# Kernel tuning notes

Hardware: AMD Instinct MI355X
Metric: run time of the kernel (lower is better)

## Reference

```python
import jax, jax.numpy as jnp
import numpy as np

B, L, DM, H = 16, 2048, 1024, 16
DK = DM // H
FACTOR = 1


def setup_inputs() -> dict:
    key = jax.random.key(0)
    ks = jax.random.split(key, 8)
    s = 0.02
    return {
        "queries": jax.random.normal(ks[0], (B, L, DM), jnp.float32),
        "keys": jax.random.normal(ks[1], (B, L, DM), jnp.float32),
        "values": jax.random.normal(ks[2], (B, L, DM), jnp.float32),
        "Wq": jax.random.normal(ks[3], (DM, DM), jnp.float32) * s,
        "Wk": jax.random.normal(ks[4], (DM, DM), jnp.float32) * s,
        "Wv": jax.random.normal(ks[5], (DM, DM), jnp.float32) * s,
        "Wo": jax.random.normal(ks[6], (DM, DM), jnp.float32) * s,
        "bo": jnp.zeros((DM,), jnp.float32),
    }


def reference(queries, keys, values, Wq, Wk, Wv, Wo, bo):
    # Projections (torch Linear: y = x @ W.T), then [B, H, DK, L] layout
    Q = (queries @ Wq.T).reshape(B, L, H, DK).transpose(0, 2, 3, 1)
    K = (keys @ Wk.T).reshape(B, L, H, DK).transpose(0, 2, 3, 1)
    V = (values @ Wv.T).reshape(B, L, H, DK).transpose(0, 2, 3, 1)

    # FFT cross-correlation along time
    qf = jnp.fft.rfft(Q, axis=-1)
    kf = jnp.fft.rfft(K, axis=-1)
    corr = jnp.fft.irfft(qf * jnp.conj(kf), n=L, axis=-1)  # [B, H, DK, L]

    # time_delay_agg_inference (eval path); B == H so torch's right-aligned
    # broadcast maps the batch axis of delay/weights onto the HEAD axis.
    top_k = int(FACTOR * np.log(L))
    mean_value = jnp.mean(corr, axis=1)                     # [B, DK, L]
    weights, delay = jax.lax.top_k(mean_value, top_k)       # [B, DK, K]
    w = jax.nn.softmax(weights, axis=-1)

    pos = jnp.arange(L)
    agg = jnp.zeros_like(V)
    for i in range(top_k):  # small fixed loop (top_k = 7)
        idx = (pos[None, None, :] + delay[:, :, i][:, :, None]) % L  # first axis aligns with H
        pattern = jnp.take_along_axis(V, jnp.broadcast_to(idx[None], V.shape), axis=-1)
        agg = agg + pattern * w[:, :, i][None, :, :, None]

    out = agg.transpose(0, 3, 1, 2).reshape(B, L, DM)  # [B, L, H*DK]
    out = out @ Wo.T + bo
    return out, corr
```

## Files before the change

### kernel.cpp

```cpp
#include <hip/hip_runtime.h>
#include <hip/hip_fp16.h>
#include <hip/hip_bf16.h>
#include <cstdint>
#include <cstddef>

typedef float  f32x4 __attribute__((ext_vector_type(4)));
typedef short  s16x8 __attribute__((ext_vector_type(8)));
typedef unsigned short u16;
typedef unsigned int   u32;
typedef u32 u32x4 __attribute__((ext_vector_type(4)));
typedef u32 u32x2 __attribute__((ext_vector_type(2)));

#define TOPK 7

__device__ __forceinline__ u32 bfpk(float re, float im) {
  __hip_bfloat162 h = __float22bfloat162_rn(make_float2(re, im));
  return *(u32*)&h;
}
__device__ __forceinline__ u16 f2bf(float f) {
  __hip_bfloat16 h = __float2bfloat16(f);
  return *(u16*)&h;
}
__device__ __forceinline__ float b2f(u16 s) {
  return __uint_as_float(((u32)s) << 16);
}
__device__ __forceinline__ float2 bfup(u32 p) {
  float2 r; r.x = b2f((u16)(p & 0xffffu)); r.y = b2f((u16)(p >> 16)); return r;
}
__device__ __forceinline__ u32 pkf16(float c, float s) {
  __half2 h = __floats2half2_rn(c, s);
  return *(u32*)&h;
}
__device__ __forceinline__ float2 upf16(u32 p) {
  __half2 h; *(u32*)&h = p;
  float2 r; r.x = __low2float(h); r.y = __high2float(h); return r;
}

typedef __attribute__((address_space(1))) void gvoid;
typedef __attribute__((address_space(3))) void lvoid;
__device__ __forceinline__ void gl_lds16(const void* g, void* l) {
  __builtin_amdgcn_global_load_lds((gvoid*)g, (lvoid*)l, 16, 0, 0);
}

__global__ void cvt_kernel(const float* __restrict__ src, u16* __restrict__ dst, int n8) {
  int i = blockIdx.x * 256 + threadIdx.x;
  if (i >= n8) return;
  const f32x4* sp = (const f32x4*)src + (size_t)i * 2;
  f32x4 a = sp[0], b = sp[1];
  u32x4 o;
  o[0] = bfpk(a[0], a[1]); o[1] = bfpk(a[2], a[3]);
  o[2] = bfpk(b[0], b[1]); o[3] = bfpk(b[2], b[3]);
  *(u32x4*)(dst + (size_t)i * 8) = o;
}

template<int MODE>
__global__ __launch_bounds__(256, 2) void gemm_bt(
    const void* __restrict__ Aptr, const u16* __restrict__ Bw,
    void* __restrict__ Cout, const float* __restrict__ bias)
{
  constexpr int K = 1024, N = 1024;
  __shared__ __align__(16) u16 lA[2][128 * 32];
  __shared__ __align__(16) u16 lB[2][128 * 32];

  int bx = blockIdx.x;
  int wg = (bx & 7) * 256 + (bx >> 3);
  int tm = wg >> 3, tn = wg & 7;
  int m0 = tm * 128, n0 = tn * 128;

  int t = threadIdx.x;
  int wid = t >> 6, lane = t & 63;
  int wm = wid >> 1, wn = wid & 1;
  int lr = lane & 15, kb = lane >> 4;

  const float* A32 = (const float*)Aptr;
  const u16*   A16 = (const u16*)Aptr;
  int r = t >> 1, half = t & 1;

  f32x4 acc[4][4] = {};

  if constexpr (MODE == 0) {
    const float* ap = A32 + (size_t)(m0 + r) * K + half * 16;
    f32x4 v[4];
#pragma unroll
    for (int g = 0; g < 4; ++g) v[g] = ((const f32x4*)ap)[g];
    u32x4 o0, o1;
    o0[0] = bfpk(v[0][0], v[0][1]); o0[1] = bfpk(v[0][2], v[0][3]);
    o0[2] = bfpk(v[1][0], v[1][1]); o0[3] = bfpk(v[1][2], v[1][3]);
    o1[0] = bfpk(v[2][0], v[2][1]); o1[1] = bfpk(v[2][2], v[2][3]);
    o1[2] = bfpk(v[3][0], v[3][1]); o1[3] = bfpk(v[3][2], v[3][3]);
    *(u32x4*)&lA[0][r * 32 + half * 16]     = o0;
    *(u32x4*)&lA[0][r * 32 + half * 16 + 8] = o1;
  } else {
#pragma unroll
    for (int it = 0; it < 2; ++it) {
      int e = (t * 16 + it * 4096) >> 1;
      gl_lds16(A16 + (size_t)(m0 + (e >> 5)) * K + (e & 31),
               (char*)&lA[0][0] + wid * 1024 + it * 4096);
    }
  }
#pragma unroll
  for (int it = 0; it < 2; ++it) {
    int e = (t * 16 + it * 4096) >> 1;
    gl_lds16(Bw + (size_t)(n0 + (e >> 5)) * K + (e & 31),
             (char*)&lB[0][0] + wid * 1024 + it * 4096);
  }
  __syncthreads();

  int cur = 0;
  for (int kt = 0; kt < 32; ++kt) {
    int nxt = cur ^ 1;
    bool pf = (kt < 31);
    f32x4 va[4];
    if (pf) {
      int k1 = (kt + 1) * 32;
      if constexpr (MODE == 0) {
        const float* ap = A32 + (size_t)(m0 + r) * K + k1 + half * 16;
#pragma unroll
        for (int g = 0; g < 4; ++g) va[g] = ((const f32x4*)ap)[g];
      } else {
#pragma unroll
        for (int it = 0; it < 2; ++it) {
          int e = (t * 16 + it * 4096) >> 1;
          gl_lds16(A16 + (size_t)(m0 + (e >> 5)) * K + k1 + (e & 31),
                   (char*)&lA[nxt][0] + wid * 1024 + it * 4096);
        }
      }
#pragma unroll
      for (int it = 0; it < 2; ++it) {
        int e = (t * 16 + it * 4096) >> 1;
        gl_lds16(Bw + (size_t)(n0 + (e >> 5)) * K + k1 + (e & 31),
                 (char*)&lB[nxt][0] + wid * 1024 + it * 4096);
      }
    }
    s16x8 af[4], bf[4];
#pragma unroll
    for (int mi = 0; mi < 4; ++mi)
      af[mi] = *(const s16x8*)&lA[cur][(wm * 64 + mi * 16 + lr) * 32 + kb * 8];
#pragma unroll
    for (int ni = 0; ni < 4; ++ni)
      bf[ni] = *(const s16x8*)&lB[cur][(wn * 64 + ni * 16 + lr) * 32 + kb * 8];
#pragma unroll
    for (int mi = 0; mi < 4; ++mi)
#pragma unroll
      for (int ni = 0; ni < 4; ++ni)
        acc[mi][ni] = __builtin_amdgcn_mfma_f32_16x16x32_bf16(af[mi], bf[ni], acc[mi][ni], 0, 0, 0);
    if (pf) {
      if constexpr (MODE == 0) {
        u32x4 o0, o1;
        o0[0] = bfpk(va[0][0], va[0][1]); o0[1] = bfpk(va[0][2], va[0][3]);
        o0[2] = bfpk(va[1][0], va[1][1]); o0[3] = bfpk(va[1][2], va[1][3]);
        o1[0] = bfpk(va[2][0], va[2][1]); o1[1] = bfpk(va[2][2], va[2][3]);
        o1[2] = bfpk(va[3][0], va[3][1]); o1[3] = bfpk(va[3][2], va[3][3]);
        *(u32x4*)&lA[nxt][r * 32 + half * 16]     = o0;
        *(u32x4*)&lA[nxt][r * 32 + half * 16 + 8] = o1;
      }
    }
    __syncthreads();
    cur = nxt;
  }

#pragma unroll
  for (int mi = 0; mi < 4; ++mi) {
    int mbase = m0 + wm * 64 + mi * 16 + kb * 4;
#pragma unroll
    for (int ni = 0; ni < 4; ++ni) {
      int nn = n0 + wn * 64 + ni * 16 + lr;
      if constexpr (MODE == 0) {
        u16* OT = (u16*)Cout;
        int b = mbase >> 11, l = mbase & 2047;
        u32x2 pk;
        pk[0] = bfpk(acc[mi][ni][0], acc[mi][ni][1]);
        pk[1] = bfpk(acc[mi][ni][2], acc[mi][ni][3]);
        *(u32x2*)(OT + ((size_t)((b << 10) + nn)) * 2048 + l) = pk;
      } else {
        float* C = (float*)Cout;
        float bv = bias[nn];
#pragma unroll
        for (int j = 0; j < 4; ++j)
          C[(size_t)(mbase + j) * N + nn] = acc[mi][ni][j] + bv;
      }
    }
  }
}


__device__ __constant__ const int BRv[32] = {
  0,16,8,24,4,20,12,28,2,18,10,26,6,22,14,30,
  1,17,9,25,5,21,13,29,3,19,11,27,7,23,15,31};
__device__ const float C32v[16] = {
  1.0f, 0.98078528f, 0.92387953f, 0.83146961f,
  0.70710678f, 0.55557023f, 0.38268343f, 0.19509032f,
  0.0f, -0.19509032f, -0.38268343f, -0.55557023f,
  -0.70710678f, -0.83146961f, -0.92387953f, -0.98078528f};
__device__ const float S32v[16] = {
  0.0f, 0.19509032f, 0.38268343f, 0.55557023f,
  0.70710678f, 0.83146961f, 0.92387953f, 0.98078528f,
  1.0f, 0.98078528f, 0.92387953f, 0.83146961f,
  0.70710678f, 0.55557023f, 0.38268343f, 0.19509032f};

#define TWIDX(j) ((j) + ((j) >> 4))

template<bool INV>
__device__ __forceinline__ void dft32(float* xr, float* xi) {
#pragma unroll
  for (int s = 0; s < 5; ++s) {
    const int half = 1 << s, step = 16 >> s;
#pragma unroll
    for (int blk = 0; blk < 32; blk += 2 * half) {
#pragma unroll
      for (int j = 0; j < half; ++j) {
        float wr = C32v[j * step];
        float wi = INV ? S32v[j * step] : -S32v[j * step];
        int p = blk + j, q = p + half;
        float vr = xr[q] * wr - xi[q] * wi;
        float vi = xr[q] * wi + xi[q] * wr;
        xr[q] = xr[p] - vr; xi[q] = xi[p] - vi;
        xr[p] = xr[p] + vr; xi[p] = xi[p] + vi;
      }
    }
  }
}

__device__ __forceinline__ void fft_fwd_row(const u32* __restrict__ zrow, int tt,
                                            u32* wsr, const u32* twp,
                                            float* xr, float* xi) {
#pragma unroll
  for (int i = 0; i < 32; ++i) {
    float2 v = bfup(zrow[32 * BRv[i] + tt]);
    xr[i] = v.x; xi[i] = v.y;
  }
  dft32<false>(xr, xi);
#pragma unroll
  for (int k1 = 0; k1 < 32; ++k1) {
    float2 w = upf16(twp[TWIDX(tt * k1)]);
    wsr[k1 * 33 + tt] = bfpk(xr[k1] * w.x - xi[k1] * w.y,
                             xr[k1] * w.y + xi[k1] * w.x);
  }
  __syncthreads();
#pragma unroll
  for (int i = 0; i < 32; ++i) {
    float2 v = bfup(wsr[tt * 33 + BRv[i]]);
    xr[i] = v.x; xi[i] = v.y;
  }
  __syncthreads();
  dft32<false>(xr, xi);
}

__device__ __forceinline__ void spec_bin(
    float zlQr, float zlQi, float zpQr, float zpQi,
    float zlKr, float zlKi, float zpKr, float zpKi,
    float wr, float wi, float& outr, float& outi)
{
  float aQr = zlQr + zpQr, aQi = zlQi - zpQi;
  float bQr = zlQr - zpQr, bQi = zlQi + zpQi;
  float gQr  = aQr + wr * bQi + wi * bQr;
  float gQi  = aQi - (wr * bQr - wi * bQi);
  float gQpr = aQr - wr * bQi - wi * bQr;
  float gQpi = -aQi - wr * bQr + wi * bQi;
  float aKr = zlKr + zpKr, aKi = zlKi - zpKi;
  float bKr = zlKr - zpKr, bKi = zlKi + zpKi;
  float gKr  = aKr + wr * bKi + wi * bKr;
  float gKi  = aKi - (wr * bKr - wi * bKi);
  float gKpr = aKr - wr * bKi - wi * bKr;
  float gKpi = -aKi - wr * bKr + wi * bKi;
  float ctr = gQr * gKr + gQi * gKi;
  float cti = gQi * gKr - gQr * gKi;
  float cpr = gQpr * gKpr + gQpi * gKpi;
  float cpi = gQpi * gKpr - gQpr * gKpi;
  float utr = ctr + cpr, uti = cti - cpi;
  float vtr = ctr - cpr, vti = cti + cpi;
  outr = (utr - wr * vti + wi * vtr) * (1.0f / 8192.0f);
  outi = (uti + wr * vtr + wi * vti) * (1.0f / 8192.0f);
}

__global__ __launch_bounds__(256) void fftcorr_kernel(
    const u16* __restrict__ Qt, const u16* __restrict__ Kt, float* __restrict__ corr)
{
  __shared__ u32 twp[1088];
  __shared__ u32 wsb[8][1056];

  int t = threadIdx.x;
#pragma unroll
  for (int i = 0; i < 4; ++i) {
    int j = t + 256 * i;
    float s, c;
    __sincosf((float)j * -6.135923151e-3f, &s, &c);
    twp[TWIDX(j)] = pkf16(c, s);
  }
  __syncthreads();

  int rl = t >> 5, tt = t & 31;
  int row = blockIdx.x * 8 + rl;
  const u32* qrow = (const u32*)Qt + (size_t)row * 1024;
  const u32* krow = (const u32*)Kt + (size_t)row * 1024;
  u32* wsr = wsb[rl];
  int lw = t & 63;
  int paddr = (((-tt) & 31) | (lw & 32)) << 2;
  bool f0 = (tt == 0);

  float xr[32], xi[32];
  u32 zkp[32], ap[32], zcp[32];

  fft_fwd_row(krow, tt, wsr, twp, xr, xi);
#pragma unroll
  for (int i = 0; i < 32; ++i) zkp[i] = bfpk(xr[i], xi[i]);
  fft_fwd_row(qrow, tt, wsr, twp, xr, xi);
#pragma unroll
  for (int i = 0; i < 32; ++i) ap[i] = bfpk(xr[i], xi[i]);

#pragma unroll
  for (int j = 0; j < 16; ++j) {
    u32 qpA = (u32)__builtin_amdgcn_ds_bpermute(paddr, (int)ap[31 - j]);
    u32 kpA = (u32)__builtin_amdgcn_ds_bpermute(paddr, (int)zkp[31 - j]);
    u32 qpB = (u32)__builtin_amdgcn_ds_bpermute(paddr, (int)ap[j]);
    u32 kpB = (u32)__builtin_amdgcn_ds_bpermute(paddr, (int)zkp[j]);
    if (f0) {
      qpA = ap[(32 - j) & 31];  kpA = zkp[(32 - j) & 31];
      qpB = ap[(j + 1) & 31];   kpB = zkp[(j + 1) & 31];
    }
    float2 bA = upf16(twp[TWIDX((tt >> 1) + 16 * j)]);
    float2 bB = upf16(twp[TWIDX((tt >> 1) + 16 * (31 - j))]);
    bool oddk = (tt & 1);
    float mr = oddk ? 0.999995293810f : 1.0f;
    float mi = oddk ? -3.067956763e-3f : 0.0f;
    float wAr = bA.x * mr - bA.y * mi, wAi = bA.x * mi + bA.y * mr;
    float wBr = bB.x * mr - bB.y * mi, wBi = bB.x * mi + bB.y * mr;
    float2 zl, zp, kl, kp;
    float or_, oi_;
    zl = bfup(ap[j]);      zp = bfup(qpA);
    kl = bfup(zkp[j]);     kp = bfup(kpA);
    spec_bin(zl.x, zl.y, zp.x, zp.y, kl.x, kl.y, kp.x, kp.y, wAr, wAi, or_, oi_);
    zcp[j] = bfpk(or_, oi_);
    zl = bfup(ap[31 - j]); zp = bfup(qpB);
    kl = bfup(zkp[31 - j]); kp = bfup(kpB);
    spec_bin(zl.x, zl.y, zp.x, zp.y, kl.x, kl.y, kp.x, kp.y, wBr, wBi, or_, oi_);
    zcp[31 - j] = bfpk(or_, oi_);
  }

#define SWPU(a, b) { u32 tp = zcp[a]; zcp[a] = zcp[b]; zcp[b] = tp; }
  SWPU(1, 16) SWPU(2, 8) SWPU(3, 24) SWPU(5, 20) SWPU(6, 12) SWPU(7, 28)
  SWPU(9, 18) SWPU(11, 26) SWPU(13, 22) SWPU(15, 30) SWPU(19, 25) SWPU(23, 29)
#undef SWPU
#pragma unroll
  for (int i = 0; i < 32; ++i) {
    float2 v = bfup(zcp[i]);
    xr[i] = v.x; xi[i] = v.y;
  }
  dft32<true>(xr, xi);
#pragma unroll
  for (int v1 = 0; v1 < 32; ++v1) {
    float2 w = upf16(twp[TWIDX(tt * v1)]);
    wsr[v1 * 33 + tt] = bfpk(xr[v1] * w.x + xi[v1] * w.y,
                             xi[v1] * w.x - xr[v1] * w.y);
  }
  __syncthreads();
#pragma unroll
  for (int i = 0; i < 32; ++i) {
    float2 v = bfup(wsr[tt * 33 + BRv[i]]);
    xr[i] = v.x; xi[i] = v.y;
  }
  dft32<true>(xr, xi);

  float2* crow = (float2*)(corr + (size_t)row * 2048);
#pragma unroll
  for (int v2 = 0; v2 < 32; ++v2) {
    float2 o; o.x = xr[v2]; o.y = xi[v2];
    crow[tt + 32 * v2] = o;
  }
}

__global__ void mean_kernel(const float* __restrict__ corr, float* __restrict__ meanp) {
  int idx = blockIdx.x * 256 + threadIdx.x;
  int l4 = idx & 511;
  int d  = (idx >> 9) & 63;
  int b  = idx >> 15;
  const f32x4* cp = (const f32x4*)corr;
  f32x4 s = {};
#pragma unroll
  for (int h = 0; h < 16; ++h)
    s += cp[((size_t)(b * 1024 + h * 64 + d)) * 512 + l4];
  ((f32x4*)meanp)[(size_t)(b * 64 + d) * 512 + l4] = s * 0.0625f;
}

__global__ __launch_bounds__(256) void topk_kernel(
    const float* __restrict__ meanp, int* __restrict__ delays, float* __restrict__ wts)
{
  int row = blockIdx.x;
  const float* mr = meanp + (size_t)row * 2048;
  int t = threadIdx.x;
  float v[8];
#pragma unroll
  for (int j = 0; j < 8; ++j) v[j] = mr[t * 8 + j];
  __shared__ float sV[256];
  __shared__ int   sI[256];
  __shared__ float topv[TOPK];
  __shared__ int   topi[TOPK];
  for (int rnd = 0; rnd < TOPK; ++rnd) {
    float bv = v[0]; int bi = t * 8;
#pragma unroll
    for (int j = 1; j < 8; ++j)
      if (v[j] > bv) { bv = v[j]; bi = t * 8 + j; }
    sV[t] = bv; sI[t] = bi;
    __syncthreads();
    for (int off = 128; off > 0; off >>= 1) {
      if (t < off) {
        float ov = sV[t + off]; int oi = sI[t + off];
        if (ov > sV[t] || (ov == sV[t] && oi < sI[t])) { sV[t] = ov; sI[t] = oi; }
      }
      __syncthreads();
    }
    int wi = sI[0];
    if (t == 0) { topv[rnd] = sV[0]; topi[rnd] = wi; }
    if ((wi >> 3) == t) {
#pragma unroll
      for (int j = 0; j < 8; ++j)
        if ((wi & 7) == j) v[j] = -__builtin_inff();
    }
    __syncthreads();
  }
  if (t == 0) {
    float mx = topv[0], sum = 0.f, e[TOPK];
#pragma unroll
    for (int i = 0; i < TOPK; ++i) { e[i] = expf(topv[i] - mx); sum += e[i]; }
#pragma unroll
    for (int i = 0; i < TOPK; ++i) {
      wts[row * 8 + i]    = e[i] / sum;
      delays[row * 8 + i] = topi[i];
    }
  }
}

__global__ __launch_bounds__(256) void agg_kernel(
    const u16* __restrict__ Vt, const float* __restrict__ wts,
    const int* __restrict__ delays, u16* __restrict__ aggt)
{
  int row = blockIdx.x;
  int c = row & 1023;
  __shared__ __align__(16) float Vs[4608];
  __shared__ float wsh[TOPK];
  __shared__ int   dsh[TOPK];
  int t = threadIdx.x;
  if (t < TOPK) { wsh[t] = wts[c * 8 + t]; dsh[t] = delays[c * 8 + t]; }
  const u16* vr = Vt + (size_t)row * 2048;
  u32x4 rv = *(const u32x4*)(vr + t * 8);
  alignas(16) u16 uv[8];
  *(u32x4*)uv = rv;
  int f0 = t * 8;
#pragma unroll
  for (int j = 0; j < 8; ++j) {
    float fv = b2f(uv[j]);
    int f  = f0 + j;
    int f2 = f + 2048;
    Vs[f  + ((f  >> 5) << 2)] = fv;
    Vs[f2 + ((f2 >> 5) << 2)] = fv;
  }
  __syncthreads();
  float o[8] = {0, 0, 0, 0, 0, 0, 0, 0};
#pragma unroll
  for (int i = 0; i < TOPK; ++i) {
    float w = wsh[i]; int dl = dsh[i];
    int base = f0 + dl;
#pragma unroll
    for (int j = 0; j < 8; ++j) {
      int f = base + j;
      o[j] += w * Vs[f + ((f >> 5) << 2)];
    }
  }
  u32x4 ob;
  ob[0] = bfpk(o[0], o[1]); ob[1] = bfpk(o[2], o[3]);
  ob[2] = bfpk(o[4], o[5]); ob[3] = bfpk(o[6], o[7]);
  *(u32x4*)(aggt + (size_t)row * 2048 + f0) = ob;
}

__global__ __launch_bounds__(256) void transpose_kernel(
    const u16* __restrict__ aggt, u16* __restrict__ aggb)
{
  int bid = blockIdx.x;
  int lt = bid & 31;
  int ct = (bid >> 5) & 15;
  int b  = bid >> 9;
  __shared__ __align__(16) u16 tile[64][72];
  int t = threadIdx.x;
  int r = t >> 2, seg = t & 3;
  const u16* src = aggt + ((size_t)(b * 1024 + ct * 64 + r)) * 2048 + lt * 64 + seg * 16;
  u32x4 v0 = *(const u32x4*)src;
  u32x4 v1 = *(const u32x4*)(src + 8);
  *(u32x4*)&tile[r][seg * 16]     = v0;
  *(u32x4*)&tile[r][seg * 16 + 8] = v1;
  __syncthreads();
  alignas(16) u16 tmp[16];
#pragma unroll
  for (int j = 0; j < 16; ++j) tmp[j] = tile[seg * 16 + j][r];
  u16* dst = aggb + ((size_t)(b * 2048 + lt * 64 + r)) * 1024 + ct * 64 + seg * 16;
  *(u32x4*)dst       = *(u32x4*)&tmp[0];
  *(u32x4*)(dst + 8) = *(u32x4*)&tmp[8];
}

extern "C" void kernel_launch(void* const* d_in, const int* in_sizes, int n_in,
                              void* d_out, int out_size, void* d_ws, size_t ws_size,
                              hipStream_t stream) {
  (void)in_sizes; (void)n_in; (void)out_size; (void)ws_size;
  const float* qin = (const float*)d_in[0];
  const float* kin = (const float*)d_in[1];
  const float* vin = (const float*)d_in[2];
  const float* Wq  = (const float*)d_in[3];
  const float* Wk  = (const float*)d_in[4];
  const float* Wv  = (const float*)d_in[5];
  const float* Wo  = (const float*)d_in[6];
  const float* bo  = (const float*)d_in[7];

  float* out  = (float*)d_out;
  float* corr = out + (size_t)33554432;

  char* ws = (char*)d_ws;
  u16* Qt  = (u16*)ws;
  u16* Kt  = (u16*)(ws + ((size_t)64  << 20));
  u16* Vt  = (u16*)(ws + ((size_t)128 << 20));
  u16* Wqb = (u16*)(ws + ((size_t)192 << 20));
  u16* Wkb = Wqb + (1u << 20);
  u16* Wvb = Wkb + (1u << 20);
  u16* Wob = Wvb + (1u << 20);
  float* meanp  = (float*)(ws + ((size_t)200 << 20));
  int*   delays = (int*)  (ws + ((size_t)208 << 20));
  float* wts    = (float*)(ws + ((size_t)208 << 20) + 65536);
  u16* aggt = Qt;
  u16* aggb = Kt;

  dim3 blk(256);
  cvt_kernel<<<512, blk, 0, stream>>>(Wq, Wqb, 131072);
  cvt_kernel<<<512, blk, 0, stream>>>(Wk, Wkb, 131072);
  cvt_kernel<<<512, blk, 0, stream>>>(Wv, Wvb, 131072);
  cvt_kernel<<<512, blk, 0, stream>>>(Wo, Wob, 131072);

  gemm_bt<0><<<2048, blk, 0, stream>>>(qin, Wqb, Qt, nullptr);
  gemm_bt<0><<<2048, blk, 0, stream>>>(kin, Wkb, Kt, nullptr);
  gemm_bt<0><<<2048, blk, 0, stream>>>(vin, Wvb, Vt, nullptr);

  fftcorr_kernel<<<2048, blk, 0, stream>>>(Qt, Kt, corr);
  mean_kernel<<<2048, blk, 0, stream>>>(corr, meanp);
  topk_kernel<<<1024, blk, 0, stream>>>(meanp, delays, wts);
  agg_kernel<<<16384, blk, 0, stream>>>(Vt, wts, delays, aggt);
  transpose_kernel<<<8192, blk, 0, stream>>>(aggt, aggb);
  gemm_bt<1><<<2048, blk, 0, stream>>>(aggb, Wob, out, bo);
}
```

Before: 762.5 us.

## Triple-buffer GEMM LDS tiles with two-stage prefetch and manual waitcnt barriers

The projection/output GEMM moves from double- to triple-buffered LDS tiles and prefetches the k-tile two iterations ahead instead of one. `__syncthreads` is replaced by explicit `s_waitcnt` vmcnt/lgkmcnt plus a raw `s_barrier`, so the newest async global-to-LDS loads can stay in flight across the barrier. Load address offsets are also hoisted out of the loop. This aims to hide more global-memory latency behind MFMA work. The cost is 50% more LDS per block, which may limit occupancy, and hand-tuned wait counts that are fragile if the compiler reorders loads.

After: 793.1 us. 1.04x slower.

```diff
diff --git a/kernel.cpp b/kernel.cpp
--- a/kernel.cpp
+++ b/kernel.cpp
@@ -59,8 +59,8 @@
     void* __restrict__ Cout, const float* __restrict__ bias)
 {
   constexpr int K = 1024, N = 1024;
-  __shared__ __align__(16) u16 lA[2][128 * 32];
-  __shared__ __align__(16) u16 lB[2][128 * 32];
+  __shared__ __align__(16) u16 lA[3][128 * 32];
+  __shared__ __align__(16) u16 lB[3][128 * 32];
 
   int bx = blockIdx.x;
   int wg = (bx & 7) * 256 + (bx >> 3);
@@ -76,61 +76,67 @@
   const u16*   A16 = (const u16*)Aptr;
   int r = t >> 1, half = t & 1;
 
+  int e0 = (t * 16) >> 1;
+  int e1 = (t * 16 + 4096) >> 1;
+  int er0 = e0 >> 5, ec0 = e0 & 31;
+  int er1 = e1 >> 5, ec1 = e1 & 31;
+
   f32x4 acc[4][4] = {};
 
+#pragma unroll
+  for (int pt = 0; pt < 2; ++pt) {
+    int k0 = pt * 32;
+    if constexpr (MODE == 0) {
+      const float* ap = A32 + (size_t)(m0 + r) * K + k0 + half * 16;
+      f32x4 v[4];
+#pragma unroll
+      for (int g = 0; g < 4; ++g) v[g] = ((const f32x4*)ap)[g];
+      u32x4 o0, o1;
+      o0[0] = bfpk(v[0][0], v[0][1]); o0[1] = bfpk(v[0][2], v[0][3]);
+      o0[2] = bfpk(v[1][0], v[1][1]); o0[3] = bfpk(v[1][2], v[1][3]);
+      o1[0] = bfpk(v[2][0], v[2][1]); o1[1] = bfpk(v[2][2], v[2][3]);
+      o1[2] = bfpk(v[3][0], v[3][1]); o1[3] = bfpk(v[3][2], v[3][3]);
+      *(u32x4*)&lA[pt][r * 32 + half * 16]     = o0;
+      *(u32x4*)&lA[pt][r * 32 + half * 16 + 8] = o1;
+    } else {
+      gl_lds16(A16 + (size_t)(m0 + er0) * K + k0 + ec0,
+               (char*)&lA[pt][0] + wid * 1024);
+      gl_lds16(A16 + (size_t)(m0 + er1) * K + k0 + ec1,
+               (char*)&lA[pt][0] + wid * 1024 + 4096);
+    }
+    gl_lds16(Bw + (size_t)(n0 + er0) * K + k0 + ec0,
+             (char*)&lB[pt][0] + wid * 1024);
+    gl_lds16(Bw + (size_t)(n0 + er1) * K + k0 + ec1,
+             (char*)&lB[pt][0] + wid * 1024 + 4096);
+  }
   if constexpr (MODE == 0) {
-    const float* ap = A32 + (size_t)(m0 + r) * K + half * 16;
-    f32x4 v[4];
-#pragma unroll
-    for (int g = 0; g < 4; ++g) v[g] = ((const f32x4*)ap)[g];
-    u32x4 o0, o1;
-    o0[0] = bfpk(v[0][0], v[0][1]); o0[1] = bfpk(v[0][2], v[0][3]);
-    o0[2] = bfpk(v[1][0], v[1][1]); o0[3] = bfpk(v[1][2], v[1][3]);
-    o1[0] = bfpk(v[2][0], v[2][1]); o1[1] = bfpk(v[2][2], v[2][3]);
-    o1[2] = bfpk(v[3][0], v[3][1]); o1[3] = bfpk(v[3][2], v[3][3]);
-    *(u32x4*)&lA[0][r * 32 + half * 16]     = o0;
-    *(u32x4*)&lA[0][r * 32 + half * 16 + 8] = o1;
+    asm volatile("s_waitcnt vmcnt(2) lgkmcnt(0)" ::: "memory");
   } else {
-#pragma unroll
-    for (int it = 0; it < 2; ++it) {
-      int e = (t * 16 + it * 4096) >> 1;
-      gl_lds16(A16 + (size_t)(m0 + (e >> 5)) * K + (e & 31),
-               (char*)&lA[0][0] + wid * 1024 + it * 4096);
-    }
-  }
-#pragma unroll
-  for (int it = 0; it < 2; ++it) {
-    int e = (t * 16 + it * 4096) >> 1;
-    gl_lds16(Bw + (size_t)(n0 + (e >> 5)) * K + (e & 31),
-             (char*)&lB[0][0] + wid * 1024 + it * 4096);
-  }
-  __syncthreads();
+    asm volatile("s_waitcnt vmcnt(4) lgkmcnt(0)" ::: "memory");
+  }
+  __builtin_amdgcn_s_barrier();
 
   int cur = 0;
   for (int kt = 0; kt < 32; ++kt) {
-    int nxt = cur ^ 1;
-    bool pf = (kt < 31);
+    int wb = cur + 2; if (wb >= 3) wb -= 3;
+    bool pf2 = (kt < 30);
     f32x4 va[4];
-    if (pf) {
-      int k1 = (kt + 1) * 32;
+    if (pf2) {
+      int k2 = (kt + 2) * 32;
       if constexpr (MODE == 0) {
-        const float* ap = A32 + (size_t)(m0 + r) * K + k1 + half * 16;
+        const float* ap = A32 + (size_t)(m0 + r) * K + k2 + half * 16;
 #pragma unroll
         for (int g = 0; g < 4; ++g) va[g] = ((const f32x4*)ap)[g];
       } else {
-#pragma unroll
-        for (int it = 0; it < 2; ++it) {
-          int e = (t * 16 + it * 4096) >> 1;
-          gl_lds16(A16 + (size_t)(m0 + (e >> 5)) * K + k1 + (e & 31),
-                   (char*)&lA[nxt][0] + wid * 1024 + it * 4096);
-        }
+        gl_lds16(A16 + (size_t)(m0 + er0) * K + k2 + ec0,
+                 (char*)&lA[wb][0] + wid * 1024);
+        gl_lds16(A16 + (size_t)(m0 + er1) * K + k2 + ec1,
+                 (char*)&lA[wb][0] + wid * 1024 + 4096);
       }
-#pragma unroll
-      for (int it = 0; it < 2; ++it) {
-        int e = (t * 16 + it * 4096) >> 1;
-        gl_lds16(Bw + (size_t)(n0 + (e >> 5)) * K + k1 + (e & 31),
-                 (char*)&lB[nxt][0] + wid * 1024 + it * 4096);
-      }
+      gl_lds16(Bw + (size_t)(n0 + er0) * K + k2 + ec0,
+               (char*)&lB[wb][0] + wid * 1024);
+      gl_lds16(Bw + (size_t)(n0 + er1) * K + k2 + ec1,
+               (char*)&lB[wb][0] + wid * 1024 + 4096);
     }
     s16x8 af[4], bf[4];
 #pragma unroll
@@ -144,19 +150,27 @@
 #pragma unroll
       for (int ni = 0; ni < 4; ++ni)
         acc[mi][ni] = __builtin_amdgcn_mfma_f32_16x16x32_bf16(af[mi], bf[ni], acc[mi][ni], 0, 0, 0);
-    if (pf) {
+    if (pf2) {
       if constexpr (MODE == 0) {
         u32x4 o0, o1;
         o0[0] = bfpk(va[0][0], va[0][1]); o0[1] = bfpk(va[0][2], va[0][3]);
         o0[2] = bfpk(va[1][0], va[1][1]); o0[3] = bfpk(va[1][2], va[1][3]);
         o1[0] = bfpk(va[2][0], va[2][1]); o1[1] = bfpk(va[2][2], va[2][3]);
         o1[2] = bfpk(va[3][0], va[3][1]); o1[3] = bfpk(va[3][2], va[3][3]);
-        *(u32x4*)&lA[nxt][r * 32 + half * 16]     = o0;
-        *(u32x4*)&lA[nxt][r * 32 + half * 16 + 8] = o1;
+        *(u32x4*)&lA[wb][r * 32 + half * 16]     = o0;
+        *(u32x4*)&lA[wb][r * 32 + half * 16 + 8] = o1;
       }
     }
-    __syncthreads();
-    cur = nxt;
+    if constexpr (MODE == 0) {
+      if (kt == 30) asm volatile("s_waitcnt vmcnt(0) lgkmcnt(0)" ::: "memory");
+      else          asm volatile("s_waitcnt lgkmcnt(0)" ::: "memory");
+    } else {
+      if (kt < 30)       asm volatile("s_waitcnt vmcnt(4) lgkmcnt(0)" ::: "memory");
+      else if (kt == 30) asm volatile("s_waitcnt vmcnt(0) lgkmcnt(0)" ::: "memory");
+      else               asm volatile("s_waitcnt lgkmcnt(0)" ::: "memory");
+    }
+    __builtin_amdgcn_s_barrier();
+    cur = cur + 1; if (cur >= 3) cur -= 3;
   }
 
 #pragma unroll
```
